# Kernel tuning notes

Measured on AMD Instinct MI355X. Metric: run time of the kernel, lower is better.

The kernel has to match this reference:

```python
import jax, jax.numpy as jnp
import numpy as np

B, L, C = 256, 197, 768
H = C // 16          # reduction = 16
N_ADAPTERS = 10
EPS = 1e-12


def l2_normalize(x, axis=-1):
    sq = jnp.sum(x * x, axis=axis, keepdims=True)
    return x * jax.lax.rsqrt(jnp.maximum(sq, EPS))


def setup_inputs() -> dict:
    key = jax.random.key(0)
    k0, k1, k2, k3 = jax.random.split(key, 4)
    x_embed = jax.random.normal(k0, (B, L, C), dtype=jnp.float32)
    # torch nn.Linear weights are [out_features, in_features]
    W1 = jax.random.normal(k1, (N_ADAPTERS, H, C), dtype=jnp.float32) * 0.02
    W2 = jax.random.normal(k2, (N_ADAPTERS, C, H), dtype=jnp.float32) * 0.02
    adapter_key = jax.random.normal(k3, (N_ADAPTERS, C), dtype=jnp.float32)
    return {"x_embed": x_embed, "W1": W1, "W2": W2, "adapter_key": adapter_key}


def reference(x_embed, W1, W2, adapter_key):
    b = x_embed.shape[0]
    # embedding_key == 'mean'
    x_mean = jnp.mean(x_embed, axis=1)                 # [B, C]
    key_norm = l2_normalize(adapter_key, axis=1)       # [10, C]
    x_norm = l2_normalize(x_mean, axis=1)              # [B, C]
    similarity = x_norm @ key_norm.T                   # [B, 10]

    # top-1 per sample, then majority vote -> single adapter id for the whole batch.
    per_sample_idx = jnp.argmax(similarity, axis=1)    # [B]
    counts = jax.ops.segment_sum(jnp.ones((b,), jnp.float32), per_sample_idx,
                                 num_segments=N_ADAPTERS)
    major = jnp.argmax(counts)                         # ties -> smallest id, matching torch
    idx = jnp.full((b, 1), major, dtype=jnp.int32)     # out['adapter_idx']

    # Apply the selected adapter (same id for every sample); len(idx[i]) == 1.
    w1 = W1[major]                                     # [H, C]
    w2 = W2[major]                                     # [C, H]
    h = jax.nn.relu(jnp.einsum('blc,hc->blh', x_embed, w1))
    a = jax.nn.relu(jnp.einsum('blh,ch->blc', h, w2))
    bias = x_embed + a                                 # (x + adapter(x)) / 1

    adapter_norm = key_norm[idx]                       # [B, 1, C]
    reduce_sim = jnp.sum(adapter_norm * x_norm[:, None, :]) / b
    return bias, reduce_sim, idx
```

## Files before the change

kernel.cpp:

```cpp
#include <hip/hip_runtime.h>
#include <hip/hip_bf16.h>

#define B_   256
#define L_   197
#define C_   768
#define H_   48
#define NA_  10
#define ROWS (B_ * L_)
#define TR   16
#define XP   776
#define HP   72
#define NBLK (ROWS / TR)
#define OFF_SIM 38731776
#define OFF_IDX 38731777
#define XBF_OFF 4876544ull
#define WS_NEED (XBF_OFF + (unsigned long long)ROWS * 1536ull)

typedef __attribute__((ext_vector_type(8))) short short8;
typedef __attribute__((ext_vector_type(4))) short short4_t;
typedef __attribute__((ext_vector_type(4))) float f32x4;

static __device__ inline short f2bf(float f) {
    union { float f; unsigned u; } v; v.f = f;
    unsigned r = v.u + 0x7fffu + ((v.u >> 16) & 1u);
    return (short)(r >> 16);
}
static __device__ inline short bfc(float f) {
    __hip_bfloat16 h = __float2bfloat16(f);
    union { __hip_bfloat16 h; short s; } u; u.h = h;
    return u.s;
}
static __device__ inline float bf2f(short s) {
    union { unsigned u; float f; } v;
    v.u = ((unsigned)(unsigned short)s) << 16;
    return v.f;
}

#define GLW(dst, p, OFF) asm volatile("global_load_dwordx4 %0, %1, off offset:" OFF \
    : "=v"(dst) : "v"(p))
#define GL2LDSB(g, l) __builtin_amdgcn_global_load_lds( \
    (const __attribute__((address_space(1))) void*)(g), \
    (__attribute__((address_space(3))) void*)(l), 16, 0, 0)

__global__ void kw_convert(const float* __restrict__ W1, const float* __restrict__ W2,
                           short* __restrict__ W1b, short* __restrict__ W2b) {
    int i = blockIdx.x * 256 + threadIdx.x;
    if (i < NA_ * H_ * C_)
        W1b[i] = f2bf(W1[i]);
    if (i < NA_ * C_ * 64) {
        int k  = i & 63;
        int nc = i >> 6;
        W2b[i] = (k < H_) ? f2bf(W2[nc * H_ + k]) : (short)0;
    }
}

__global__ void pre_sum_cast(const float* __restrict__ x, float* __restrict__ partial,
                             short* __restrict__ xbf) {
    int b = blockIdx.x >> 2, seg = blockIdx.x & 3;
    int l0 = seg * 50, l1 = l0 + 50; if (l1 > L_) l1 = L_;
    int t = threadIdx.x;
    const float* xb = x + (size_t)b * L_ * C_ + t * 4;
    char* xbfb = (char*)xbf;
    float4 s = {0.f, 0.f, 0.f, 0.f};
    for (int l = l0; l < l1; ++l) {
        float4 v = *(const float4*)(xb + (size_t)l * C_);
        s.x += v.x; s.y += v.y; s.z += v.z; s.w += v.w;
        size_t R = (size_t)b * L_ + l;
        short4_t sb;
        sb[0] = bfc(v.x); sb[1] = bfc(v.y); sb[2] = bfc(v.z); sb[3] = bfc(v.w);
        unsigned cb = ((unsigned)t * 8) ^ (((unsigned)R & 7u) << 4);
        *(short4_t*)(xbfb + R * 1536 + cb) = sb;
    }
    float* p = partial + ((size_t)b * 4 + seg) * C_ + t * 4;
    *(float4*)p = s;
}

__global__ void k1a_partial(const float* __restrict__ x, float* __restrict__ partial) {
    int b = blockIdx.x >> 2, seg = blockIdx.x & 3;
    int l0 = seg * 50, l1 = l0 + 50; if (l1 > L_) l1 = L_;
    int t = threadIdx.x;
    const float* xb = x + (size_t)b * L_ * C_ + t * 4;
    float4 s = {0.f, 0.f, 0.f, 0.f};
    #pragma unroll 5
    for (int l = l0; l < l1; ++l) {
        float4 v = *(const float4*)(xb + (size_t)l * C_);
        s.x += v.x; s.y += v.y; s.z += v.z; s.w += v.w;
    }
    *(float4*)(partial + ((size_t)b * 4 + seg) * C_ + t * 4) = s;
}

__global__ void k1b_sims(const float* __restrict__ partial, const float* __restrict__ akey,
                         float* __restrict__ sims) {
    __shared__ float red[21][256];
    int b = blockIdx.x, t = threadIdx.x;
    const float* p = partial + (size_t)b * 4 * C_;
    float m[3];
    #pragma unroll
    for (int j = 0; j < 3; ++j) {
        int c = t + j * 256;
        m[j] = (p[c] + p[C_ + c] + p[2 * C_ + c] + p[3 * C_ + c]) * (1.f / (float)L_);
    }
    red[0][t] = m[0] * m[0] + m[1] * m[1] + m[2] * m[2];
    #pragma unroll
    for (int k = 0; k < NA_; ++k) {
        float kd = 0.f, kq = 0.f;
        #pragma unroll
        for (int j = 0; j < 3; ++j) {
            float kv = akey[k * C_ + t + j * 256];
            kd += m[j] * kv; kq += kv * kv;
        }
        red[1 + k][t] = kd; red[11 + k][t] = kq;
    }
    __syncthreads();
    for (int s = 128; s > 0; s >>= 1) {
        if (t < s) {
            #pragma unroll
            for (int q = 0; q < 21; ++q) red[q][t] += red[q][t + s];
        }
        __syncthreads();
    }
    if (t < NA_) {
        float msq = red[0][0];
        sims[b * NA_ + t] = red[1 + t][0] * rsqrtf(fmaxf(red[11 + t][0], 1e-12f))
                                          * rsqrtf(fmaxf(msq, 1e-12f));
    }
}

__global__ void k2_select(const float* __restrict__ sims, float* __restrict__ out,
                          int* __restrict__ majorp) {
    __shared__ int counts[NA_];
    __shared__ int majorS;
    __shared__ float rs[256];
    int t = threadIdx.x;
    float s[NA_];
    #pragma unroll
    for (int k = 0; k < NA_; ++k) s[k] = sims[t * NA_ + k];
    int best = 0; float bv = s[0];
    #pragma unroll
    for (int k = 1; k < NA_; ++k) { if (s[k] > bv) { bv = s[k]; best = k; } }
    if (t < NA_) counts[t] = 0;
    __syncthreads();
    atomicAdd(&counts[best], 1);
    __syncthreads();
    if (t == 0) {
        int mj = 0, mc = counts[0];
        #pragma unroll
        for (int k = 1; k < NA_; ++k) { if (counts[k] > mc) { mc = counts[k]; mj = k; } }
        majorS = mj; *majorp = mj;
    }
    __syncthreads();
    int mj = majorS;
    rs[t] = s[mj];
    __syncthreads();
    for (int st = 128; st > 0; st >>= 1) { if (t < st) rs[t] += rs[t + st]; __syncthreads(); }
    if (t == 0) out[OFF_SIM] = rs[0] * (1.f / (float)B_);
    out[OFF_IDX + t] = (float)mj;
}

__launch_bounds__(192, 2)
__global__ void k3b_apply(const short* __restrict__ xbf, const short* __restrict__ W1b,
                          const short* __restrict__ W2b, const int* __restrict__ majorp,
                          float* __restrict__ out) {
    __shared__ short xs[TR * 768];
    __shared__ short hs[TR * HP];
    const int major = *majorp;

    int t = threadIdx.x;
    int w = t >> 6, l = t & 63;
    int rbase = blockIdx.x * TR;
    int lo16 = l & 15;
    int g = l >> 4;
    int klane = g * 8;
    const int swz = (lo16 & 7) << 4;

    {
        const char* src = (const char*)xbf + (size_t)rbase * 1536 + (size_t)l * 16;
        char* dst = (char*)xs;
        #pragma unroll
        for (int j = 0; j < 8; ++j)
            GL2LDSB(src + (w * 8 + j) * 1024, dst + (w * 8 + j) * 1024);
    }
    __syncthreads();

    {
        const short* w1p = W1b + major * (H_ * C_) + (size_t)(w * 16 + lo16) * C_ + klane;
        f32x4 acc = {0, 0, 0, 0};
        short8 q0, q1, q2, q3, q4, q5, q6, q7, q8, q9, q10, q11;
        short8 q12, q13, q14, q15, q16, q17, q18, q19, q20, q21, q22, q23;

#define G1STEP(KK, Q) { \
        short8 xa = *(const short8*)((const char*)xs + lo16 * 1536 + (((KK) * 64 + g * 16) ^ swz)); \
        acc = __builtin_amdgcn_mfma_f32_16x16x32_bf16(xa, Q, acc, 0, 0, 0); }

        GLW(q0,  w1p, "0");    GLW(q1,  w1p, "64");   GLW(q2,  w1p, "128");
        GLW(q3,  w1p, "192");  GLW(q4,  w1p, "256");  GLW(q5,  w1p, "320");
        GLW(q6,  w1p, "384");  GLW(q7,  w1p, "448");  GLW(q8,  w1p, "512");
        GLW(q9,  w1p, "576");  GLW(q10, w1p, "640");  GLW(q11, w1p, "704");
        GLW(q12, w1p, "768");  GLW(q13, w1p, "832");  GLW(q14, w1p, "896");
        GLW(q15, w1p, "960");  GLW(q16, w1p, "1024"); GLW(q17, w1p, "1088");
        GLW(q18, w1p, "1152"); GLW(q19, w1p, "1216"); GLW(q20, w1p, "1280");
        GLW(q21, w1p, "1344"); GLW(q22, w1p, "1408"); GLW(q23, w1p, "1472");
        asm volatile("s_waitcnt vmcnt(12)"
            : "+v"(q0), "+v"(q1), "+v"(q2), "+v"(q3), "+v"(q4), "+v"(q5),
              "+v"(q6), "+v"(q7), "+v"(q8), "+v"(q9), "+v"(q10), "+v"(q11));
        __builtin_amdgcn_sched_barrier(0);
        G1STEP(0, q0)  G1STEP(1, q1)  G1STEP(2, q2)  G1STEP(3, q3)
        G1STEP(4, q4)  G1STEP(5, q5)  G1STEP(6, q6)  G1STEP(7, q7)
        G1STEP(8, q8)  G1STEP(9, q9)  G1STEP(10, q10) G1STEP(11, q11)
        asm volatile("s_waitcnt vmcnt(0)"
            : "+v"(q12), "+v"(q13), "+v"(q14), "+v"(q15), "+v"(q16), "+v"(q17),
              "+v"(q18), "+v"(q19), "+v"(q20), "+v"(q21), "+v"(q22), "+v"(q23));
        __builtin_amdgcn_sched_barrier(0);
        G1STEP(12, q12) G1STEP(13, q13) G1STEP(14, q14) G1STEP(15, q15)
        G1STEP(16, q16) G1STEP(17, q17) G1STEP(18, q18) G1STEP(19, q19)
        G1STEP(20, q20) G1STEP(21, q21) G1STEP(22, q22) G1STEP(23, q23)
#undef G1STEP

        #pragma unroll
        for (int q = 0; q < 4; ++q)
            hs[(g * 4 + q) * HP + w * 16 + lo16] = bfc(fmaxf(acc[q], 0.f));
        if (w == 0) {
            short4_t z = {0, 0, 0, 0};
            *(short4_t*)&hs[lo16 * HP + 48 + g * 4] = z;
        }
    }

    {
        const short* ba = W2b + (size_t)major * (C_ * 64)
                              + (size_t)(w * 16) * 1024 + lo16 * 64 + klane;
        const short* b1 = ba + 2048;
        const short* b2 = ba + 4096;
        const short* b3 = ba + 6144;
        const short* b4 = ba + 8192;
        const short* b5 = ba + 10240;
        const short* b6 = ba + 12288;
        const short* b7 = ba + 14336;
        short8 p0a, p0b, p1a, p1b, p2a, p2b, p3a, p3b;
        short8 p4a, p4b, p5a, p5b, p6a, p6b, p7a, p7b;
        short8 p8a, p8b, p9a, p9b, p10a, p10b, p11a, p11b;
        short8 p12a, p12b, p13a, p13b, p14a, p14b, p15a, p15b;

        GLW(p0a,  ba, "0");    GLW(p0b,  ba, "64");
        GLW(p1a,  ba, "2048"); GLW(p1b,  ba, "2112");
        GLW(p2a,  b1, "0");    GLW(p2b,  b1, "64");
        GLW(p3a,  b1, "2048"); GLW(p3b,  b1, "2112");
        GLW(p4a,  b2, "0");    GLW(p4b,  b2, "64");
        GLW(p5a,  b2, "2048"); GLW(p5b,  b2, "2112");
        GLW(p6a,  b3, "0");    GLW(p6b,  b3, "64");
        GLW(p7a,  b3, "2048"); GLW(p7b,  b3, "2112");
        GLW(p8a,  b4, "0");    GLW(p8b,  b4, "64");
        GLW(p9a,  b4, "2048"); GLW(p9b,  b4, "2112");
        GLW(p10a, b5, "0");    GLW(p10b, b5, "64");
        GLW(p11a, b5, "2048"); GLW(p11b, b5, "2112");
        GLW(p12a, b6, "0");    GLW(p12b, b6, "64");
        GLW(p13a, b6, "2048"); GLW(p13b, b6, "2112");
        GLW(p14a, b7, "0");    GLW(p14b, b7, "64");
        GLW(p15a, b7, "2048"); GLW(p15b, b7, "2112");

        __syncthreads();

        short8 hA = *(const short8*)&hs[lo16 * HP + klane];
        short8 hB = *(const short8*)&hs[lo16 * HP + 32 + klane];
        float* outr = out + (size_t)(rbase + lo16) * C_ + w * 256 + g * 4;

#define G2STEP(JJ, P0, P1) { \
        f32x4 acc = {0, 0, 0, 0}; \
        acc = __builtin_amdgcn_mfma_f32_16x16x32_bf16(P0, hA, acc, 0, 0, 0); \
        acc = __builtin_amdgcn_mfma_f32_16x16x32_bf16(P1, hB, acc, 0, 0, 0); \
        short4_t xbv = *(const short4_t*)((const char*)xs + lo16 * 1536 + \
                         ((w * 512 + (JJ) * 32 + g * 8) ^ swz)); \
        f32x4 ov; \
        ov[0] = bf2f(xbv[0]) + fmaxf(acc[0], 0.f); \
        ov[1] = bf2f(xbv[1]) + fmaxf(acc[1], 0.f); \
        ov[2] = bf2f(xbv[2]) + fmaxf(acc[2], 0.f); \
        ov[3] = bf2f(xbv[3]) + fmaxf(acc[3], 0.f); \
        *(f32x4*)(outr + (JJ) * 16) = ov; }

        asm volatile("s_waitcnt vmcnt(16)"
            : "+v"(p0a), "+v"(p0b), "+v"(p1a), "+v"(p1b),
              "+v"(p2a), "+v"(p2b), "+v"(p3a), "+v"(p3b),
              "+v"(p4a), "+v"(p4b), "+v"(p5a), "+v"(p5b),
              "+v"(p6a), "+v"(p6b), "+v"(p7a), "+v"(p7b));
        __builtin_amdgcn_sched_barrier(0);
        G2STEP(0, p0a, p0b)   G2STEP(1, p1a, p1b)
        G2STEP(2, p2a, p2b)   G2STEP(3, p3a, p3b)
        G2STEP(4, p4a, p4b)   G2STEP(5, p5a, p5b)
        G2STEP(6, p6a, p6b)   G2STEP(7, p7a, p7b)
        asm volatile("s_waitcnt vmcnt(8)"
            : "+v"(p8a), "+v"(p8b), "+v"(p9a), "+v"(p9b),
              "+v"(p10a), "+v"(p10b), "+v"(p11a), "+v"(p11b),
              "+v"(p12a), "+v"(p12b), "+v"(p13a), "+v"(p13b),
              "+v"(p14a), "+v"(p14b), "+v"(p15a), "+v"(p15b));
        __builtin_amdgcn_sched_barrier(0);
        G2STEP(8, p8a, p8b)   G2STEP(9, p9a, p9b)
        G2STEP(10, p10a, p10b) G2STEP(11, p11a, p11b)
        G2STEP(12, p12a, p12b) G2STEP(13, p13a, p13b)
        G2STEP(14, p14a, p14b) G2STEP(15, p15a, p15b)
#undef G2STEP
    }
}

__launch_bounds__(192, 2)
__global__ void k3_apply(const float* __restrict__ x, const short* __restrict__ W1b,
                         const short* __restrict__ W2b, const int* __restrict__ majorp,
                         float* __restrict__ out) {
    __shared__ short xs[TR * XP];
    __shared__ short hs[TR * HP];
    const int major = *majorp;
    int t = threadIdx.x;
    int w = t >> 6, l = t & 63;
    int rbase = blockIdx.x * TR;
    int lo16 = l & 15;
    int g = l >> 4;
    int klane = g * 8;
    {
        const float* xsrc = x + (size_t)rbase * C_ + t * 4;
        const float* c0 = xsrc;
        const float* c1 = xsrc + 2 * C_;
        const float* c2 = xsrc + 4 * C_;
        const float* c3 = xsrc + 6 * C_;
        const float* c4 = xsrc + 8 * C_;
        const float* c5 = xsrc + 10 * C_;
        const float* c6 = xsrc + 12 * C_;
        const float* c7 = xsrc + 14 * C_;
        f32x4 v0, v1, v2, v3, v4, v5, v6, v7, v8, v9, v10, v11, v12, v13, v14, v15;
        GLW(v0,  c0, "0"); GLW(v1,  c0, "3072");
        GLW(v2,  c1, "0"); GLW(v3,  c1, "3072");
        GLW(v4,  c2, "0"); GLW(v5,  c2, "3072");
        GLW(v6,  c3, "0"); GLW(v7,  c3, "3072");
        GLW(v8,  c4, "0"); GLW(v9,  c4, "3072");
        GLW(v10, c5, "0"); GLW(v11, c5, "3072");
        GLW(v12, c6, "0"); GLW(v13, c6, "3072");
        GLW(v14, c7, "0"); GLW(v15, c7, "3072");
#define STROW(ROW, V) { \
        short4_t sb; \
        sb[0] = bfc((V)[0]); sb[1] = bfc((V)[1]); \
        sb[2] = bfc((V)[2]); sb[3] = bfc((V)[3]); \
        *(short4_t*)&xs[(ROW) * XP + t * 4] = sb; }
        asm volatile("s_waitcnt vmcnt(8)"
            : "+v"(v0), "+v"(v1), "+v"(v2), "+v"(v3),
              "+v"(v4), "+v"(v5), "+v"(v6), "+v"(v7));
        __builtin_amdgcn_sched_barrier(0);
        STROW(0, v0) STROW(1, v1) STROW(2, v2) STROW(3, v3)
        STROW(4, v4) STROW(5, v5) STROW(6, v6) STROW(7, v7)
        asm volatile("s_waitcnt vmcnt(0)"
            : "+v"(v8), "+v"(v9), "+v"(v10), "+v"(v11),
              "+v"(v12), "+v"(v13), "+v"(v14), "+v"(v15));
        __builtin_amdgcn_sched_barrier(0);
        STROW(8, v8)   STROW(9, v9)   STROW(10, v10) STROW(11, v11)
        STROW(12, v12) STROW(13, v13) STROW(14, v14) STROW(15, v15)
#undef STROW
    }
    __syncthreads();
    {
        const short* w1p = W1b + major * (H_ * C_) + (size_t)(w * 16 + lo16) * C_ + klane;
        f32x4 acc = {0, 0, 0, 0};
        short8 q0, q1, q2, q3, q4, q5, q6, q7, q8, q9, q10, q11;
        short8 q12, q13, q14, q15, q16, q17, q18, q19, q20, q21, q22, q23;
#define G1STEP(KK, Q) { \
        short8 xa = *(const short8*)&xs[lo16 * XP + (KK) * 32 + klane]; \
        acc = __builtin_amdgcn_mfma_f32_16x16x32_bf16(xa, Q, acc, 0, 0, 0); }
        GLW(q0,  w1p, "0");    GLW(q1,  w1p, "64");   GLW(q2,  w1p, "128");
        GLW(q3,  w1p, "192");  GLW(q4,  w1p, "256");  GLW(q5,  w1p, "320");
        GLW(q6,  w1p, "384");  GLW(q7,  w1p, "448");  GLW(q8,  w1p, "512");
        GLW(q9,  w1p, "576");  GLW(q10, w1p, "640");  GLW(q11, w1p, "704");
        GLW(q12, w1p, "768");  GLW(q13, w1p, "832");  GLW(q14, w1p, "896");
        GLW(q15, w1p, "960");  GLW(q16, w1p, "1024"); GLW(q17, w1p, "1088");
        GLW(q18, w1p, "1152"); GLW(q19, w1p, "1216"); GLW(q20, w1p, "1280");
        GLW(q21, w1p, "1344"); GLW(q22, w1p, "1408"); GLW(q23, w1p, "1472");
        asm volatile("s_waitcnt vmcnt(12)"
            : "+v"(q0), "+v"(q1), "+v"(q2), "+v"(q3), "+v"(q4), "+v"(q5),
              "+v"(q6), "+v"(q7), "+v"(q8), "+v"(q9), "+v"(q10), "+v"(q11));
        __builtin_amdgcn_sched_barrier(0);
        G1STEP(0, q0)  G1STEP(1, q1)  G1STEP(2, q2)  G1STEP(3, q3)
        G1STEP(4, q4)  G1STEP(5, q5)  G1STEP(6, q6)  G1STEP(7, q7)
        G1STEP(8, q8)  G1STEP(9, q9)  G1STEP(10, q10) G1STEP(11, q11)
        asm volatile("s_waitcnt vmcnt(0)"
            : "+v"(q12), "+v"(q13), "+v"(q14), "+v"(q15), "+v"(q16), "+v"(q17),
              "+v"(q18), "+v"(q19), "+v"(q20), "+v"(q21), "+v"(q22), "+v"(q23));
        __builtin_amdgcn_sched_barrier(0);
        G1STEP(12, q12) G1STEP(13, q13) G1STEP(14, q14) G1STEP(15, q15)
        G1STEP(16, q16) G1STEP(17, q17) G1STEP(18, q18) G1STEP(19, q19)
        G1STEP(20, q20) G1STEP(21, q21) G1STEP(22, q22) G1STEP(23, q23)
#undef G1STEP
        #pragma unroll
        for (int q = 0; q < 4; ++q)
            hs[(g * 4 + q) * HP + w * 16 + lo16] = bfc(fmaxf(acc[q], 0.f));
        if (w == 0) {
            short4_t z = {0, 0, 0, 0};
            *(short4_t*)&hs[lo16 * HP + 48 + g * 4] = z;
        }
    }
    __syncthreads();
    {
        short8 hA = *(const short8*)&hs[lo16 * HP + klane];
        short8 hB = *(const short8*)&hs[lo16 * HP + 32 + klane];
        const short* ba = W2b + (size_t)major * (C_ * 64)
                              + (size_t)(w * 16) * 1024 + lo16 * 64 + klane;
        const short* d1 = ba + 2048;
        const short* d2 = ba + 4096;
        const short* d3 = ba + 6144;
        const short* d4 = ba + 8192;
        const short* d5 = ba + 10240;
        const short* d6 = ba + 12288;
        const short* d7 = ba + 14336;
        short8 p0a, p0b, p1a, p1b, p2a, p2b, p3a, p3b;
        short8 p4a, p4b, p5a, p5b, p6a, p6b, p7a, p7b;
        short8 p8a, p8b, p9a, p9b, p10a, p10b, p11a, p11b;
        short8 p12a, p12b, p13a, p13b, p14a, p14b, p15a, p15b;
        GLW(p0a,  ba, "0");    GLW(p0b,  ba, "64");
        GLW(p1a,  ba, "2048"); GLW(p1b,  ba, "2112");
        GLW(p2a,  d1, "0");    GLW(p2b,  d1, "64");
        GLW(p3a,  d1, "2048"); GLW(p3b,  d1, "2112");
        GLW(p4a,  d2, "0");    GLW(p4b,  d2, "64");
        GLW(p5a,  d2, "2048"); GLW(p5b,  d2, "2112");
        GLW(p6a,  d3, "0");    GLW(p6b,  d3, "64");
        GLW(p7a,  d3, "2048"); GLW(p7b,  d3, "2112");
        GLW(p8a,  d4, "0");    GLW(p8b,  d4, "64");
        GLW(p9a,  d4, "2048"); GLW(p9b,  d4, "2112");
        GLW(p10a, d5, "0");    GLW(p10b, d5, "64");
        GLW(p11a, d5, "2048"); GLW(p11b, d5, "2112");
        GLW(p12a, d6, "0");    GLW(p12b, d6, "64");
        GLW(p13a, d6, "2048"); GLW(p13b, d6, "2112");
        GLW(p14a, d7, "0");    GLW(p14b, d7, "64");
        GLW(p15a, d7, "2048"); GLW(p15b, d7, "2112");
        float* outr = out + (size_t)(rbase + lo16) * C_ + w * 256 + g * 4;
#define G2STEP(JJ, P0, P1) { \
        f32x4 acc = {0, 0, 0, 0}; \
        acc = __builtin_amdgcn_mfma_f32_16x16x32_bf16(P0, hA, acc, 0, 0, 0); \
        acc = __builtin_amdgcn_mfma_f32_16x16x32_bf16(P1, hB, acc, 0, 0, 0); \
        short4_t xbv = *(const short4_t*)&xs[lo16 * XP + (w * 16 + (JJ)) * 16 + g * 4]; \
        f32x4 ov; \
        ov[0] = bf2f(xbv[0]) + fmaxf(acc[0], 0.f); \
        ov[1] = bf2f(xbv[1]) + fmaxf(acc[1], 0.f); \
        ov[2] = bf2f(xbv[2]) + fmaxf(acc[2], 0.f); \
        ov[3] = bf2f(xbv[3]) + fmaxf(acc[3], 0.f); \
        *(f32x4*)(outr + (JJ) * 16) = ov; }
        asm volatile("s_waitcnt vmcnt(16)"
            : "+v"(p0a), "+v"(p0b), "+v"(p1a), "+v"(p1b),
              "+v"(p2a), "+v"(p2b), "+v"(p3a), "+v"(p3b),
              "+v"(p4a), "+v"(p4b), "+v"(p5a), "+v"(p5b),
              "+v"(p6a), "+v"(p6b), "+v"(p7a), "+v"(p7b));
        __builtin_amdgcn_sched_barrier(0);
        G2STEP(0, p0a, p0b)   G2STEP(1, p1a, p1b)
        G2STEP(2, p2a, p2b)   G2STEP(3, p3a, p3b)
        G2STEP(4, p4a, p4b)   G2STEP(5, p5a, p5b)
        G2STEP(6, p6a, p6b)   G2STEP(7, p7a, p7b)
        asm volatile("s_waitcnt vmcnt(8)"
            : "+v"(p8a), "+v"(p8b), "+v"(p9a), "+v"(p9b),
              "+v"(p10a), "+v"(p10b), "+v"(p11a), "+v"(p11b),
              "+v"(p12a), "+v"(p12b), "+v"(p13a), "+v"(p13b),
              "+v"(p14a), "+v"(p14b), "+v"(p15a), "+v"(p15b));
        __builtin_amdgcn_sched_barrier(0);
        G2STEP(8, p8a, p8b)   G2STEP(9, p9a, p9b)
        G2STEP(10, p10a, p10b) G2STEP(11, p11a, p11b)
        G2STEP(12, p12a, p12b) G2STEP(13, p13a, p13b)
        G2STEP(14, p14a, p14b) G2STEP(15, p15a, p15b)
#undef G2STEP
    }
}

extern "C" void kernel_launch(void* const* d_in, const int* in_sizes, int n_in,
                              void* d_out, int out_size, void* d_ws, size_t ws_size,
                              hipStream_t stream) {
    const float* x    = (const float*)d_in[0];
    const float* W1   = (const float*)d_in[1];
    const float* W2   = (const float*)d_in[2];
    const float* akey = (const float*)d_in[3];
    float* out = (float*)d_out;

    char* ws = (char*)d_ws;
    short* W1b     = (short*)ws;
    short* W2b     = (short*)(ws + 737280);
    float* partial = (float*)(ws + 1720320);
    float* sims    = (float*)(ws + 4866048);
    int*   majorp  = (int*)(ws + 4876288);
    short* xbf     = (short*)(ws + XBF_OFF);

    hipLaunchKernelGGL(kw_convert, dim3(1920), dim3(256), 0, stream, W1, W2, W1b, W2b);
    if (ws_size >= WS_NEED) {
        hipLaunchKernelGGL(pre_sum_cast, dim3(B_ * 4), dim3(192), 0, stream, x, partial, xbf);
        hipLaunchKernelGGL(k1b_sims, dim3(B_), dim3(256), 0, stream, partial, akey, sims);
        hipLaunchKernelGGL(k2_select, dim3(1), dim3(256), 0, stream, sims, out, majorp);
        hipLaunchKernelGGL(k3b_apply, dim3(NBLK), dim3(192), 0, stream, xbf, W1b, W2b, majorp, out);
    } else {
        hipLaunchKernelGGL(k1a_partial, dim3(B_ * 4), dim3(192), 0, stream, x, partial);
        hipLaunchKernelGGL(k1b_sims, dim3(B_), dim3(256), 0, stream, partial, akey, sims);
        hipLaunchKernelGGL(k2_select, dim3(1), dim3(256), 0, stream, sims, out, majorp);
        hipLaunchKernelGGL(k3_apply, dim3(NBLK), dim3(192), 0, stream, x, W1b, W2b, majorp, out);
    }
}
```

Measured before the change: 148.3 us.

## Make apply kernel persistent over four row tiles with double-buffered LDS prefetch

The apply kernel now handles four consecutive 16-row tiles per block instead of one, with the launch grid shrunk to match. The next tile's bf16 activations are prefetched into a second LDS buffer while the current tile runs its two MFMA stages, so the global-to-LDS latency can hide behind compute. The pre-pass summation loop also gains an unroll pragma. In exchange the kernel uses twice the LDS for activations, adds an extra barrier per tile, reloads the weight fragments for every tile, and has fewer blocks to spread across CUs.

```diff
diff --git a/kernel.cpp b/kernel.cpp
--- a/kernel.cpp
+++ b/kernel.cpp
@@ -11,6 +11,8 @@
 #define XP   776
 #define HP   72
 #define NBLK (ROWS / TR)
+#define PT   4
+#define GBLK (NBLK / PT)
 #define OFF_SIM 38731776
 #define OFF_IDX 38731777
 #define XBF_OFF 4876544ull
@@ -62,6 +64,7 @@
     const float* xb = x + (size_t)b * L_ * C_ + t * 4;
     char* xbfb = (char*)xbf;
     float4 s = {0.f, 0.f, 0.f, 0.f};
+    #pragma unroll 5
     for (int l = l0; l < l1; ++l) {
         float4 v = *(const float4*)(xb + (size_t)l * C_);
         s.x += v.x; s.y += v.y; s.z += v.z; s.w += v.w;
@@ -71,8 +74,7 @@
         unsigned cb = ((unsigned)t * 8) ^ (((unsigned)R & 7u) << 4);
         *(short4_t*)(xbfb + R * 1536 + cb) = sb;
     }
-    float* p = partial + ((size_t)b * 4 + seg) * C_ + t * 4;
-    *(float4*)p = s;
+    *(float4*)(partial + ((size_t)b * 4 + seg) * C_ + t * 4) = s;
 }
 
 __global__ void k1a_partial(const float* __restrict__ x, float* __restrict__ partial) {
@@ -158,40 +160,50 @@
 }
 
 __launch_bounds__(192, 2)
-__global__ void k3b_apply(const short* __restrict__ xbf, const short* __restrict__ W1b,
+__global__ void k3c_apply(const short* __restrict__ xbf, const short* __restrict__ W1b,
                           const short* __restrict__ W2b, const int* __restrict__ majorp,
                           float* __restrict__ out) {
-    __shared__ short xs[TR * 768];
+    __shared__ short xs[2][TR * 768];
     __shared__ short hs[TR * HP];
     const int major = *majorp;
 
     int t = threadIdx.x;
     int w = t >> 6, l = t & 63;
-    int rbase = blockIdx.x * TR;
     int lo16 = l & 15;
     int g = l >> 4;
     int klane = g * 8;
     const int swz = (lo16 & 7) << 4;
+    const char* xbfB = (const char*)xbf;
+
+    if (w == 0) {
+        short4_t z = {0, 0, 0, 0};
+        *(short4_t*)&hs[lo16 * HP + 48 + g * 4] = z;
+    }
 
     {
-        const char* src = (const char*)xbf + (size_t)rbase * 1536 + (size_t)l * 16;
-        char* dst = (char*)xs;
+        const char* src = xbfB + (size_t)(blockIdx.x * PT) * TR * 1536 + (size_t)l * 16;
+        char* dst = (char*)&xs[0][0];
         #pragma unroll
         for (int j = 0; j < 8; ++j)
             GL2LDSB(src + (w * 8 + j) * 1024, dst + (w * 8 + j) * 1024);
     }
-    __syncthreads();
-
-    {
-        const short* w1p = W1b + major * (H_ * C_) + (size_t)(w * 16 + lo16) * C_ + klane;
-        f32x4 acc = {0, 0, 0, 0};
+    asm volatile("s_waitcnt vmcnt(0)");
+    __builtin_amdgcn_sched_barrier(0);
+    __syncthreads();
+
+    const short* w1p = W1b + major * (H_ * C_) + (size_t)(w * 16 + lo16) * C_ + klane;
+    const short* w2b0 = W2b + (size_t)major * (C_ * 64)
+                            + (size_t)(w * 16) * 1024 + lo16 * 64 + klane;
+
+    #pragma unroll
+    for (int p = 0; p < PT; ++p) {
+        const int cur = p & 1;
+        const int nxt = cur ^ 1;
+        const int rbase = (blockIdx.x * PT + p) * TR;
+        const char* xcur = (const char*)&xs[cur][0];
+
         short8 q0, q1, q2, q3, q4, q5, q6, q7, q8, q9, q10, q11;
         short8 q12, q13, q14, q15, q16, q17, q18, q19, q20, q21, q22, q23;
-
-#define G1STEP(KK, Q) { \
-        short8 xa = *(const short8*)((const char*)xs + lo16 * 1536 + (((KK) * 64 + g * 16) ^ swz)); \
-        acc = __builtin_amdgcn_mfma_f32_16x16x32_bf16(xa, Q, acc, 0, 0, 0); }
-
         GLW(q0,  w1p, "0");    GLW(q1,  w1p, "64");   GLW(q2,  w1p, "128");
         GLW(q3,  w1p, "192");  GLW(q4,  w1p, "256");  GLW(q5,  w1p, "320");
         GLW(q6,  w1p, "384");  GLW(q7,  w1p, "448");  GLW(q8,  w1p, "512");
@@ -200,17 +212,34 @@
         GLW(q15, w1p, "960");  GLW(q16, w1p, "1024"); GLW(q17, w1p, "1088");
         GLW(q18, w1p, "1152"); GLW(q19, w1p, "1216"); GLW(q20, w1p, "1280");
         GLW(q21, w1p, "1344"); GLW(q22, w1p, "1408"); GLW(q23, w1p, "1472");
-        asm volatile("s_waitcnt vmcnt(12)"
-            : "+v"(q0), "+v"(q1), "+v"(q2), "+v"(q3), "+v"(q4), "+v"(q5),
-              "+v"(q6), "+v"(q7), "+v"(q8), "+v"(q9), "+v"(q10), "+v"(q11));
-        __builtin_amdgcn_sched_barrier(0);
+
+        if (p < PT - 1) {
+            const char* src = xbfB + (size_t)(rbase + TR) * 1536 + (size_t)l * 16;
+            char* dst = (char*)&xs[nxt][0];
+            #pragma unroll
+            for (int j = 0; j < 8; ++j)
+                GL2LDSB(src + (w * 8 + j) * 1024, dst + (w * 8 + j) * 1024);
+            asm volatile("s_waitcnt vmcnt(8)"
+                : "+v"(q0), "+v"(q1), "+v"(q2), "+v"(q3), "+v"(q4), "+v"(q5),
+                  "+v"(q6), "+v"(q7), "+v"(q8), "+v"(q9), "+v"(q10), "+v"(q11),
+                  "+v"(q12), "+v"(q13), "+v"(q14), "+v"(q15), "+v"(q16), "+v"(q17),
+                  "+v"(q18), "+v"(q19), "+v"(q20), "+v"(q21), "+v"(q22), "+v"(q23));
+        } else {
+            asm volatile("s_waitcnt vmcnt(0)"
+                : "+v"(q0), "+v"(q1), "+v"(q2), "+v"(q3), "+v"(q4), "+v"(q5),
+                  "+v"(q6), "+v"(q7), "+v"(q8), "+v"(q9), "+v"(q10), "+v"(q11),
+                  "+v"(q12), "+v"(q13), "+v"(q14), "+v"(q15), "+v"(q16), "+v"(q17),
+                  "+v"(q18), "+v"(q19), "+v"(q20), "+v"(q21), "+v"(q22), "+v"(q23));
+        }
+        __builtin_amdgcn_sched_barrier(0);
+
+        f32x4 acc = {0, 0, 0, 0};
+#define G1STEP(KK, Q) { \
+        short8 xa = *(const short8*)(xcur + lo16 * 1536 + (((KK) * 64 + g * 16) ^ swz)); \
+        acc = __builtin_amdgcn_mfma_f32_16x16x32_bf16(xa, Q, acc, 0, 0, 0); }
         G1STEP(0, q0)  G1STEP(1, q1)  G1STEP(2, q2)  G1STEP(3, q3)
         G1STEP(4, q4)  G1STEP(5, q5)  G1STEP(6, q6)  G1STEP(7, q7)
         G1STEP(8, q8)  G1STEP(9, q9)  G1STEP(10, q10) G1STEP(11, q11)
-        asm volatile("s_waitcnt vmcnt(0)"
-            : "+v"(q12), "+v"(q13), "+v"(q14), "+v"(q15), "+v"(q16), "+v"(q17),
-              "+v"(q18), "+v"(q19), "+v"(q20), "+v"(q21), "+v"(q22), "+v"(q23));
-        __builtin_amdgcn_sched_barrier(0);
         G1STEP(12, q12) G1STEP(13, q13) G1STEP(14, q14) G1STEP(15, q15)
         G1STEP(16, q16) G1STEP(17, q17) G1STEP(18, q18) G1STEP(19, q19)
         G1STEP(20, q20) G1STEP(21, q21) G1STEP(22, q22) G1STEP(23, q23)
@@ -219,43 +248,34 @@
         #pragma unroll
         for (int q = 0; q < 4; ++q)
             hs[(g * 4 + q) * HP + w * 16 + lo16] = bfc(fmaxf(acc[q], 0.f));
-        if (w == 0) {
-            short4_t z = {0, 0, 0, 0};
-            *(short4_t*)&hs[lo16 * HP + 48 + g * 4] = z;
-        }
-    }
-
-    {
-        const short* ba = W2b + (size_t)major * (C_ * 64)
-                              + (size_t)(w * 16) * 1024 + lo16 * 64 + klane;
-        const short* b1 = ba + 2048;
-        const short* b2 = ba + 4096;
-        const short* b3 = ba + 6144;
-        const short* b4 = ba + 8192;
-        const short* b5 = ba + 10240;
-        const short* b6 = ba + 12288;
-        const short* b7 = ba + 14336;
+
+        const short* d1 = w2b0 + 2048;
+        const short* d2 = w2b0 + 4096;
+        const short* d3 = w2b0 + 6144;
+        const short* d4 = w2b0 + 8192;
+        const short* d5 = w2b0 + 10240;
+        const short* d6 = w2b0 + 12288;
+        const short* d7 = w2b0 + 14336;
         short8 p0a, p0b, p1a, p1b, p2a, p2b, p3a, p3b;
         short8 p4a, p4b, p5a, p5b, p6a, p6b, p7a, p7b;
         short8 p8a, p8b, p9a, p9b, p10a, p10b, p11a, p11b;
         short8 p12a, p12b, p13a, p13b, p14a, p14b, p15a, p15b;
-
-        GLW(p0a,  ba, "0");    GLW(p0b,  ba, "64");
-        GLW(p1a,  ba, "2048"); GLW(p1b,  ba, "2112");
-        GLW(p2a,  b1, "0");    GLW(p2b,  b1, "64");
-        GLW(p3a,  b1, "2048"); GLW(p3b,  b1, "2112");
-        GLW(p4a,  b2, "0");    GLW(p4b,  b2, "64");
-        GLW(p5a,  b2, "2048"); GLW(p5b,  b2, "2112");
-        GLW(p6a,  b3, "0");    GLW(p6b,  b3, "64");
-        GLW(p7a,  b3, "2048"); GLW(p7b,  b3, "2112");
-        GLW(p8a,  b4, "0");    GLW(p8b,  b4, "64");
-        GLW(p9a,  b4, "2048"); GLW(p9b,  b4, "2112");
-        GLW(p10a, b5, "0");    GLW(p10b, b5, "64");
-        GLW(p11a, b5, "2048"); GLW(p11b, b5, "2112");
-        GLW(p12a, b6, "0");    GLW(p12b, b6, "64");
-        GLW(p13a, b6, "2048"); GLW(p13b, b6, "2112");
-        GLW(p14a, b7, "0");    GLW(p14b, b7, "64");
-        GLW(p15a, b7, "2048"); GLW(p15b, b7, "2112");
+        GLW(p0a,  w2b0, "0");    GLW(p0b,  w2b0, "64");
+        GLW(p1a,  w2b0, "2048"); GLW(p1b,  w2b0, "2112");
+        GLW(p2a,  d1, "0");    GLW(p2b,  d1, "64");
+        GLW(p3a,  d1, "2048"); GLW(p3b,  d1, "2112");
+        GLW(p4a,  d2, "0");    GLW(p4b,  d2, "64");
+        GLW(p5a,  d2, "2048"); GLW(p5b,  d2, "2112");
+        GLW(p6a,  d3, "0");    GLW(p6b,  d3, "64");
+        GLW(p7a,  d3, "2048"); GLW(p7b,  d3, "2112");
+        GLW(p8a,  d4, "0");    GLW(p8b,  d4, "64");
+        GLW(p9a,  d4, "2048"); GLW(p9b,  d4, "2112");
+        GLW(p10a, d5, "0");    GLW(p10b, d5, "64");
+        GLW(p11a, d5, "2048"); GLW(p11b, d5, "2112");
+        GLW(p12a, d6, "0");    GLW(p12b, d6, "64");
+        GLW(p13a, d6, "2048"); GLW(p13b, d6, "2112");
+        GLW(p14a, d7, "0");    GLW(p14b, d7, "64");
+        GLW(p15a, d7, "2048"); GLW(p15b, d7, "2112");
 
         __syncthreads();
 
@@ -264,16 +284,16 @@
         float* outr = out + (size_t)(rbase + lo16) * C_ + w * 256 + g * 4;
 
 #define G2STEP(JJ, P0, P1) { \
-        f32x4 acc = {0, 0, 0, 0}; \
-        acc = __builtin_amdgcn_mfma_f32_16x16x32_bf16(P0, hA, acc, 0, 0, 0); \
-        acc = __builtin_amdgcn_mfma_f32_16x16x32_bf16(P1, hB, acc, 0, 0, 0); \
-        short4_t xbv = *(const short4_t*)((const char*)xs + lo16 * 1536 + \
+        f32x4 a2 = {0, 0, 0, 0}; \
+        a2 = __builtin_amdgcn_mfma_f32_16x16x32_bf16(P0, hA, a2, 0, 0, 0); \
+        a2 = __builtin_amdgcn_mfma_f32_16x16x32_bf16(P1, hB, a2, 0, 0, 0); \
+        short4_t xbv = *(const short4_t*)(xcur + lo16 * 1536 + \
                          ((w * 512 + (JJ) * 32 + g * 8) ^ swz)); \
         f32x4 ov; \
-        ov[0] = bf2f(xbv[0]) + fmaxf(acc[0], 0.f); \
-        ov[1] = bf2f(xbv[1]) + fmaxf(acc[1], 0.f); \
-        ov[2] = bf2f(xbv[2]) + fmaxf(acc[2], 0.f); \
-        ov[3] = bf2f(xbv[3]) + fmaxf(acc[3], 0.f); \
+        ov[0] = bf2f(xbv[0]) + fmaxf(a2[0], 0.f); \
+        ov[1] = bf2f(xbv[1]) + fmaxf(a2[1], 0.f); \
+        ov[2] = bf2f(xbv[2]) + fmaxf(a2[2], 0.f); \
+        ov[3] = bf2f(xbv[3]) + fmaxf(a2[3], 0.f); \
         *(f32x4*)(outr + (JJ) * 16) = ov; }
 
         asm volatile("s_waitcnt vmcnt(16)"
@@ -297,6 +317,8 @@
         G2STEP(12, p12a, p12b) G2STEP(13, p13a, p13b)
         G2STEP(14, p14a, p14b) G2STEP(15, p15a, p15b)
 #undef G2STEP
+
+        __syncthreads();
     }
 }
 
@@ -426,15 +448,15 @@
         GLW(p15a, d7, "2048"); GLW(p15b, d7, "2112");
         float* outr = out + (size_t)(rbase + lo16) * C_ + w * 256 + g * 4;
 #define G2STEP(JJ, P0, P1) { \
-        f32x4 acc = {0, 0, 0, 0}; \
-        acc = __builtin_amdgcn_mfma_f32_16x16x32_bf16(P0, hA, acc, 0, 0, 0); \
-        acc = __builtin_amdgcn_mfma_f32_16x16x32_bf16(P1, hB, acc, 0, 0, 0); \
+        f32x4 a2 = {0, 0, 0, 0}; \
+        a2 = __builtin_amdgcn_mfma_f32_16x16x32_bf16(P0, hA, a2, 0, 0, 0); \
+        a2 = __builtin_amdgcn_mfma_f32_16x16x32_bf16(P1, hB, a2, 0, 0, 0); \
         short4_t xbv = *(const short4_t*)&xs[lo16 * XP + (w * 16 + (JJ)) * 16 + g * 4]; \
         f32x4 ov; \
-        ov[0] = bf2f(xbv[0]) + fmaxf(acc[0], 0.f); \
-        ov[1] = bf2f(xbv[1]) + fmaxf(acc[1], 0.f); \
-        ov[2] = bf2f(xbv[2]) + fmaxf(acc[2], 0.f); \
-        ov[3] = bf2f(xbv[3]) + fmaxf(acc[3], 0.f); \
+        ov[0] = bf2f(xbv[0]) + fmaxf(a2[0], 0.f); \
+        ov[1] = bf2f(xbv[1]) + fmaxf(a2[1], 0.f); \
+        ov[2] = bf2f(xbv[2]) + fmaxf(a2[2], 0.f); \
+        ov[3] = bf2f(xbv[3]) + fmaxf(a2[3], 0.f); \
         *(f32x4*)(outr + (JJ) * 16) = ov; }
         asm volatile("s_waitcnt vmcnt(16)"
             : "+v"(p0a), "+v"(p0b), "+v"(p1a), "+v"(p1b),
@@ -482,7 +504,7 @@
         hipLaunchKernelGGL(pre_sum_cast, dim3(B_ * 4), dim3(192), 0, stream, x, partial, xbf);
         hipLaunchKernelGGL(k1b_sims, dim3(B_), dim3(256), 0, stream, partial, akey, sims);
         hipLaunchKernelGGL(k2_select, dim3(1), dim3(256), 0, stream, sims, out, majorp);
-        hipLaunchKernelGGL(k3b_apply, dim3(NBLK), dim3(192), 0, stream, xbf, W1b, W2b, majorp, out);
+        hipLaunchKernelGGL(k3c_apply, dim3(GBLK), dim3(192), 0, stream, xbf, W1b, W2b, majorp, out);
     } else {
         hipLaunchKernelGGL(k1a_partial, dim3(B_ * 4), dim3(192), 0, stream, x, partial);
         hipLaunchKernelGGL(k1b_sims, dim3(B_), dim3(256), 0, stream, partial, akey, sims);
```

Measured after the change: 167.8 us. 13.2% more time.
